# Kernel tuning notes

Hardware: AMD Instinct MI355X
Metric: run time of the kernel (lower is better)

The kernel has to match this reference:

```python
import jax, jax.numpy as jnp
import numpy as np

N_NODES = 100000
N_EDGES = 600000
NUM_GRAPHS = 512
IN_DIM = 128
HID = 64
HEADS = 2
NEG_SLOPE = 0.2


def gat_layer(h_in, src, dst, W, a_s, a_d, b, n_nodes):
    # W: [F_in, H*C], a_s/a_d: [H, C], b: [H*C]
    H, C = a_s.shape
    h = (h_in @ W).reshape(n_nodes, H, C)            # [N,H,C]
    alpha_src = jnp.einsum('nhc,hc->nh', h, a_s)      # [N,H]
    alpha_dst = jnp.einsum('nhc,hc->nh', h, a_d)      # [N,H]
    e = alpha_src[src] + alpha_dst[dst]               # [E,H]
    e = jnp.where(e >= 0, e, NEG_SLOPE * e)           # leaky_relu
    # segment softmax over destination node
    m = jax.ops.segment_max(e, dst, num_segments=n_nodes)
    m = jnp.where(jnp.isfinite(m), m, 0.0)
    ex = jnp.exp(e - m[dst])                          # [E,H]
    denom = jax.ops.segment_sum(ex, dst, num_segments=n_nodes)
    alpha = ex / jnp.maximum(denom[dst], 1e-16)       # [E,H]
    out = jax.ops.segment_sum(alpha[:, :, None] * h[src], dst, num_segments=n_nodes)
    return out.reshape(n_nodes, H * C) + b


def setup_inputs() -> dict:
    key = jax.random.key(0)
    ks = jax.random.split(key, 16)
    x = jax.random.normal(ks[0], (N_NODES, IN_DIM), dtype=jnp.float32)
    edge_index = jax.random.randint(ks[1], (2, N_EDGES), 0, N_NODES, dtype=jnp.int32)
    batch = jnp.sort(jax.random.randint(ks[2], (N_NODES,), 0, NUM_GRAPHS, dtype=jnp.int32))
    s = lambda *d: 1.0 / np.sqrt(d[0])
    W1 = jax.random.normal(ks[3], (IN_DIM, HEADS * HID), jnp.float32) * s(IN_DIM)
    a_src1 = jax.random.normal(ks[4], (HEADS, HID), jnp.float32) * s(HID)
    a_dst1 = jax.random.normal(ks[5], (HEADS, HID), jnp.float32) * s(HID)
    b1 = jnp.zeros((HEADS * HID,), jnp.float32)
    W2 = jax.random.normal(ks[6], (HEADS * HID, HID), jnp.float32) * s(HEADS * HID)
    a_src2 = jax.random.normal(ks[7], (1, HID), jnp.float32) * s(HID)
    a_dst2 = jax.random.normal(ks[8], (1, HID), jnp.float32) * s(HID)
    b2 = jnp.zeros((HID,), jnp.float32)
    Wf1 = jax.random.normal(ks[9], (2 * HID, HID), jnp.float32) * s(2 * HID)
    bf1 = jnp.zeros((HID,), jnp.float32)
    Wf2 = jax.random.normal(ks[10], (HID, 1), jnp.float32) * s(HID)
    bf2 = jnp.zeros((1,), jnp.float32)
    return dict(x=x, edge_index=edge_index, batch=batch, W1=W1, a_src1=a_src1,
                a_dst1=a_dst1, b1=b1, W2=W2, a_src2=a_src2, a_dst2=a_dst2, b2=b2,
                Wf1=Wf1, bf1=bf1, Wf2=Wf2, bf2=bf2)


def reference(x, edge_index, batch, W1, a_src1, a_dst1, b1, W2, a_src2, a_dst2, b2,
              Wf1, bf1, Wf2, bf2):
    n = x.shape[0]
    loops = jnp.arange(n, dtype=edge_index.dtype)
    src = jnp.concatenate([edge_index[0], loops])
    dst = jnp.concatenate([edge_index[1], loops])
    h = gat_layer(x, src, dst, W1, a_src1, a_dst1, b1, n)
    h = jax.nn.relu(h)
    h = gat_layer(h, src, dst, W2, a_src2, a_dst2, b2, n)  # [N, HID]
    # global mean + max pool per graph
    ones = jnp.ones((n,), h.dtype)
    counts = jax.ops.segment_sum(ones, batch, num_segments=NUM_GRAPHS)  # [G]
    mean = jax.ops.segment_sum(h, batch, num_segments=NUM_GRAPHS) / jnp.maximum(counts, 1.0)[:, None]
    mx = jax.ops.segment_max(h, batch, num_segments=NUM_GRAPHS)
    mx = jnp.where(counts[:, None] > 0, mx, 0.0)
    pooled = jnp.concatenate([mean, mx], axis=1)  # [G, 2*HID]
    out = jax.nn.relu(pooled @ Wf1 + bf1) @ Wf2 + bf2  # [G, 1]
    return out
```

## Files before the change

### kernel.cpp

```cpp
#include <hip/hip_runtime.h>

#define N_NODESC 100000
#define N_EDGESC 600000
#define E_TOTC   700000
#define NUM_GRAPHSC 512
#define NEG_SLOPE 0.2f
#define NEG_INF_ENC 0x007FFFFFu
#define SCAN_NB 128

typedef unsigned short ushort_t;
typedef __attribute__((ext_vector_type(8))) short bf16x8;
typedef __attribute__((ext_vector_type(4))) float f32x4;

__device__ __forceinline__ unsigned enc_f32(float f) {
    unsigned u = __float_as_uint(f);
    return (u & 0x80000000u) ? ~u : (u | 0x80000000u);
}
__device__ __forceinline__ float dec_f32(unsigned u) {
    u = (u & 0x80000000u) ? (u ^ 0x80000000u) : ~u;
    return __uint_as_float(u);
}
__device__ __forceinline__ ushort_t f32_to_bf16(float f) {
    unsigned u = __float_as_uint(f);
    return (ushort_t)((u + 0x7FFFu + ((u >> 16) & 1u)) >> 16);
}
__device__ __forceinline__ float bf16_to_f32(ushort_t h) {
    return __uint_as_float(((unsigned)h) << 16);
}
__device__ __forceinline__ unsigned pack_bf16x2(float a, float b) {
    return (unsigned)f32_to_bf16(a) | ((unsigned)f32_to_bf16(b) << 16);
}

__global__ __launch_bounds__(256) void init_all(float* __restrict__ msum,
                                                unsigned* __restrict__ mmax,
                                                float* __restrict__ cnt,
                                                int* __restrict__ deg,
                                                const float* __restrict__ W1,
                                                const float* __restrict__ W2,
                                                ushort_t* __restrict__ wPre1,
                                                ushort_t* __restrict__ wPre2) {
    int i = blockIdx.x * 256 + threadIdx.x;
    if (i < NUM_GRAPHSC * 64) { msum[i] = 0.f; mmax[i] = NEG_INF_ENC; }
    if (i < NUM_GRAPHSC) cnt[i] = 0.f;
    if (i < N_NODESC) deg[i] = 0;
    if (i < 128 * 128) {
        int n = i >> 7, k = i & 127;
        wPre1[n * 128 + k] = f32_to_bf16(W1[k * 128 + n]);
    } else if (i < 128 * 128 + 64 * 128) {
        int j = i - 128 * 128;
        int n = j >> 7, k = j & 127;
        wPre2[n * 128 + k] = f32_to_bf16(W2[k * 64 + n]);
    }
}

__global__ __launch_bounds__(256) void hist_dst(const int* __restrict__ ei,
                                                int* __restrict__ deg) {
    int e = blockIdx.x * blockDim.x + threadIdx.x;
    if (e >= E_TOTC) return;
    int d = (e < N_EDGESC) ? ei[N_EDGESC + e] : e - N_EDGESC;
    atomicAdd(&deg[d], 1);
}

__global__ __launch_bounds__(256) void scan_partial(const int* __restrict__ deg,
                                                    int* __restrict__ bsum, int n) {
    __shared__ int red[256];
    int chunk = (n + SCAN_NB - 1) / SCAN_NB;
    int lo = blockIdx.x * chunk, hi = min(lo + chunk, n);
    int s = 0;
    for (int i = lo + threadIdx.x; i < hi; i += 256) s += deg[i];
    red[threadIdx.x] = s;
    __syncthreads();
    for (int d = 128; d; d >>= 1) {
        if (threadIdx.x < d) red[threadIdx.x] += red[threadIdx.x + d];
        __syncthreads();
    }
    if (threadIdx.x == 0) bsum[blockIdx.x] = red[0];
}

__global__ __launch_bounds__(256) void scan_final(const int* __restrict__ deg,
                                                  const int* __restrict__ bsum,
                                                  int* __restrict__ off, int n) {
    __shared__ int bs[SCAN_NB];
    __shared__ int tile[256];
    __shared__ int carry;
    int t = threadIdx.x;
    if (t < SCAN_NB) bs[t] = bsum[t];
    __syncthreads();
    for (int d = 1; d < SCAN_NB; d <<= 1) {
        int v = (t >= d && t < SCAN_NB) ? bs[t - d] : 0;
        __syncthreads();
        if (t < SCAN_NB) bs[t] += v;
        __syncthreads();
    }
    if (t == 0) carry = blockIdx.x ? bs[blockIdx.x - 1] : 0;
    __syncthreads();
    int chunk = (n + SCAN_NB - 1) / SCAN_NB;
    int lo = blockIdx.x * chunk, hi = min(lo + chunk, n);
    for (int base = lo; base < hi; base += 256) {
        int i = base + t;
        int v = (i < hi) ? deg[i] : 0;
        tile[t] = v;
        __syncthreads();
        for (int d = 1; d < 256; d <<= 1) {
            int u = (t >= d) ? tile[t - d] : 0;
            __syncthreads();
            tile[t] += u;
            __syncthreads();
        }
        if (i < hi) off[i] = carry + tile[t] - v;
        __syncthreads();
        if (t == 0) carry += tile[255];
        __syncthreads();
    }
}

__global__ __launch_bounds__(256) void scatter_csr(const int* __restrict__ ei,
                                                   int* __restrict__ off,
                                                   int* __restrict__ csr) {
    int e = blockIdx.x * blockDim.x + threadIdx.x;
    if (e >= E_TOTC) return;
    int s, d;
    if (e < N_EDGESC) { s = ei[e]; d = ei[N_EDGESC + e]; } else { s = d = e - N_EDGESC; }
    int slot = atomicAdd(&off[d], 1);
    csr[slot] = s;
}

__global__ __launch_bounds__(256) void gemm1_mfma(const float* __restrict__ X,
                                                  const ushort_t* __restrict__ Wp,
                                                  ushort_t* __restrict__ Y16, int N) {
    int tid = threadIdx.x;
    int wave = tid >> 6, lane = tid & 63;
    int quad = lane >> 4, l16 = lane & 15;
    size_t node0 = (size_t)blockIdx.x * 64 + wave * 16;

    size_t arow = node0 + l16;
    if (arow >= (size_t)N) arow = N - 1;
    const float* xp = X + arow * 128;
    float4 xa[4], xb[4];
#pragma unroll
    for (int kc = 0; kc < 4; ++kc) {
        xa[kc] = *(const float4*)(xp + kc * 32 + quad * 8);
        xb[kc] = *(const float4*)(xp + kc * 32 + quad * 8 + 4);
    }

    f32x4 acc[8];
#pragma unroll
    for (int ct = 0; ct < 8; ++ct) acc[ct] = (f32x4){0.f, 0.f, 0.f, 0.f};

#pragma unroll
    for (int kc = 0; kc < 4; ++kc) {
        int kb = kc * 32 + quad * 8;
        union { bf16x8 v; unsigned u[4]; } af;
        af.u[0] = pack_bf16x2(xa[kc].x, xa[kc].y);
        af.u[1] = pack_bf16x2(xa[kc].z, xa[kc].w);
        af.u[2] = pack_bf16x2(xb[kc].x, xb[kc].y);
        af.u[3] = pack_bf16x2(xb[kc].z, xb[kc].w);
#pragma unroll
        for (int ct = 0; ct < 8; ++ct) {
            bf16x8 b = *(const bf16x8*)(Wp + (size_t)(ct * 16 + l16) * 128 + kb);
            acc[ct] = __builtin_amdgcn_mfma_f32_16x16x32_bf16(af.v, b, acc[ct], 0, 0, 0);
        }
    }
    unsigned* Yu = (unsigned*)Y16;
#pragma unroll
    for (int ct = 0; ct < 4; ++ct) {
        int c = ct * 16 + l16;
#pragma unroll
        for (int r = 0; r < 4; ++r) {
            size_t row = node0 + quad * 4 + r;
            if (row < (size_t)N)
                Yu[row * 64 + c] = pack_bf16x2(acc[ct][r], acc[ct + 4][r]);
        }
    }
}

__global__ __launch_bounds__(256) void gemm2_mfma(const ushort_t* __restrict__ Xb,
                                                  const ushort_t* __restrict__ Wp,
                                                  ushort_t* __restrict__ Y16, int N) {
    int tid = threadIdx.x;
    int wave = tid >> 6, lane = tid & 63;
    int quad = lane >> 4, l16 = lane & 15;
    int rbase = (wave >> 1) * 32, cbase = (wave & 1) * 32;
    size_t node0 = (size_t)blockIdx.x * 64;

    bf16x8 a[2][4];
#pragma unroll
    for (int rt = 0; rt < 2; ++rt) {
        size_t row = node0 + rbase + rt * 16 + l16;
        if (row >= (size_t)N) row = N - 1;
#pragma unroll
        for (int kc = 0; kc < 4; ++kc)
            a[rt][kc] = *(const bf16x8*)(Xb + row * 128 + kc * 32 + quad * 8);
    }

    const ushort_t* b0p = Wp + (size_t)(cbase + l16) * 128;
    const ushort_t* b1p = Wp + (size_t)(cbase + 16 + l16) * 128;

    f32x4 acc[2][2];
#pragma unroll
    for (int rt = 0; rt < 2; ++rt)
#pragma unroll
        for (int ct = 0; ct < 2; ++ct) acc[rt][ct] = (f32x4){0.f, 0.f, 0.f, 0.f};

#pragma unroll
    for (int kc = 0; kc < 4; ++kc) {
        int kb = kc * 32 + quad * 8;
        bf16x8 b0 = *(const bf16x8*)(b0p + kb);
        bf16x8 b1 = *(const bf16x8*)(b1p + kb);
#pragma unroll
        for (int rt = 0; rt < 2; ++rt) {
            acc[rt][0] = __builtin_amdgcn_mfma_f32_16x16x32_bf16(a[rt][kc], b0, acc[rt][0], 0, 0, 0);
            acc[rt][1] = __builtin_amdgcn_mfma_f32_16x16x32_bf16(a[rt][kc], b1, acc[rt][1], 0, 0, 0);
        }
    }
#pragma unroll
    for (int rt = 0; rt < 2; ++rt)
#pragma unroll
        for (int ct = 0; ct < 2; ++ct)
#pragma unroll
            for (int r = 0; r < 4; ++r) {
                size_t row = node0 + rbase + rt * 16 + quad * 4 + r;
                if (row < (size_t)N)
                    Y16[row * 64 + cbase + ct * 16 + l16] = f32_to_bf16(acc[rt][ct][r]);
            }
}

template <int H>
__global__ __launch_bounds__(256) void node_alpha(const ushort_t* __restrict__ H16,
                                                  const float* __restrict__ a_s,
                                                  const float* __restrict__ a_d,
                                                  float* __restrict__ as_out,
                                                  float* __restrict__ ad_out, int N) {
    int wid = threadIdx.x >> 6, lane = threadIdx.x & 63;
    int n = blockIdx.x * 4 + wid;
    if (n >= N) return;
    if (H == 2) {
        const unsigned* hrow = (const unsigned*)(H16 + (size_t)n * 128);
        unsigned u = hrow[lane];
        float h0 = __uint_as_float(u << 16);
        float h1 = __uint_as_float(u & 0xffff0000u);
        float ps0 = h0 * a_s[lane], pd0 = h0 * a_d[lane];
        float ps1 = h1 * a_s[64 + lane], pd1 = h1 * a_d[64 + lane];
#pragma unroll
        for (int off = 32; off; off >>= 1) {
            ps0 += __shfl_xor(ps0, off);
            pd0 += __shfl_xor(pd0, off);
            ps1 += __shfl_xor(ps1, off);
            pd1 += __shfl_xor(pd1, off);
        }
        if (lane == 0) {
            as_out[n * 2 + 0] = ps0; ad_out[n * 2 + 0] = pd0;
            as_out[n * 2 + 1] = ps1; ad_out[n * 2 + 1] = pd1;
        }
    } else {
        float hv = bf16_to_f32(H16[(size_t)n * 64 + lane]);
        float ps = hv * a_s[lane];
        float pd = hv * a_d[lane];
#pragma unroll
        for (int off = 32; off; off >>= 1) {
            ps += __shfl_xor(ps, off);
            pd += __shfl_xor(pd, off);
        }
        if (lane == 0) { as_out[n] = ps; ad_out[n] = pd; }
    }
}

template <int H, bool RELU, bool OB16>
__global__ __launch_bounds__(256) void gat_gather(const int* __restrict__ off_end,
                                                  const int* __restrict__ deg,
                                                  const int* __restrict__ csr,
                                                  const float* __restrict__ as,
                                                  const float* __restrict__ ad,
                                                  const ushort_t* __restrict__ H16,
                                                  const float* __restrict__ b,
                                                  void* __restrict__ outp, int N) {
    int lane = threadIdx.x & 63;
    int wave = threadIdx.x >> 6;
    int l = lane & 15;
    int gbase = lane & 48;
    int n = blockIdx.x * 16 + wave * 4 + (lane >> 4);
    if (n >= N) return;
    int dg = deg[n];
    int o = off_end[n] - dg;
    float adv[H];
#pragma unroll
    for (int h = 0; h < H; ++h) adv[h] = ad[n * H + h];

    float acc[H][4], den[H];
#pragma unroll
    for (int h = 0; h < H; ++h) {
        den[h] = 0.f;
#pragma unroll
        for (int q = 0; q < 4; ++q) acc[h][q] = 0.f;
    }

    const unsigned* Hu = (const unsigned*)H16;

    for (int base = 0; base < dg; base += 16) {
        int i = base + l;
        bool valid = i < dg;
        int s = valid ? csr[o + i] : 0;
        float v[H];
        if (H == 2) {
            float2 p = valid ? ((const float2*)as)[s] : make_float2(0.f, 0.f);
            v[0] = p.x + adv[0];
            v[H - 1] = p.y + adv[H - 1];
        } else {
            v[0] = valid ? as[s] + adv[0] : 0.f;
        }
#pragma unroll
        for (int h = 0; h < H; ++h) {
            float e = v[h] >= 0.f ? v[h] : NEG_SLOPE * v[h];
            v[h] = valid ? __expf(e) : 0.f;
            den[h] += v[h];
        }
        int wpk = (H == 2) ? (int)pack_bf16x2(v[0], v[H - 1])
                           : (int)__float_as_uint(v[0]);
        int cnt = min(dg - base, 16);
        int cnt4 = (cnt + 3) & ~3;
        for (int j = 0; j < cnt4; j += 4) {
#pragma unroll
            for (int u = 0; u < 4; ++u) {
                int src = gbase + j + u;
                int sj = __shfl(s, src);
                int wp = __shfl(wpk, src);
                if (H == 2) {
                    float w0 = __uint_as_float(((unsigned)wp) << 16);
                    float w1 = __uint_as_float(((unsigned)wp) & 0xffff0000u);
                    uint4 hu = *(const uint4*)(Hu + (size_t)sj * 64 + l * 4);
                    acc[0][0] += w0 * __uint_as_float(hu.x << 16);
                    acc[H - 1][0] += w1 * __uint_as_float(hu.x & 0xffff0000u);
                    acc[0][1] += w0 * __uint_as_float(hu.y << 16);
                    acc[H - 1][1] += w1 * __uint_as_float(hu.y & 0xffff0000u);
                    acc[0][2] += w0 * __uint_as_float(hu.z << 16);
                    acc[H - 1][2] += w1 * __uint_as_float(hu.z & 0xffff0000u);
                    acc[0][3] += w0 * __uint_as_float(hu.w << 16);
                    acc[H - 1][3] += w1 * __uint_as_float(hu.w & 0xffff0000u);
                } else {
                    float w0 = __uint_as_float((unsigned)wp);
                    uint2 hu = *(const uint2*)((const unsigned*)(H16 + (size_t)sj * 64) + l * 2);
                    acc[0][0] += w0 * __uint_as_float(hu.x << 16);
                    acc[0][1] += w0 * __uint_as_float(hu.x & 0xffff0000u);
                    acc[0][2] += w0 * __uint_as_float(hu.y << 16);
                    acc[0][3] += w0 * __uint_as_float(hu.y & 0xffff0000u);
                }
            }
        }
    }
#pragma unroll
    for (int h = 0; h < H; ++h) {
#pragma unroll
        for (int sh = 8; sh; sh >>= 1) den[h] += __shfl_xor(den[h], sh);
    }
    if (H == 2) {
        float4 b0 = *(const float4*)(b + l * 4);
        float4 b1 = *(const float4*)(b + 64 + l * 4);
        float r0[4], r1[4];
        float id0 = 1.f / fmaxf(den[0], 1e-16f);
        float id1 = 1.f / fmaxf(den[H - 1], 1e-16f);
        r0[0] = acc[0][0] * id0 + b0.x; r0[1] = acc[0][1] * id0 + b0.y;
        r0[2] = acc[0][2] * id0 + b0.z; r0[3] = acc[0][3] * id0 + b0.w;
        r1[0] = acc[H - 1][0] * id1 + b1.x; r1[1] = acc[H - 1][1] * id1 + b1.y;
        r1[2] = acc[H - 1][2] * id1 + b1.z; r1[3] = acc[H - 1][3] * id1 + b1.w;
        if (RELU) {
#pragma unroll
            for (int q = 0; q < 4; ++q) { r0[q] = fmaxf(r0[q], 0.f); r1[q] = fmaxf(r1[q], 0.f); }
        }
        ushort_t* outb = (ushort_t*)outp;
        uint2 p0 = make_uint2(pack_bf16x2(r0[0], r0[1]), pack_bf16x2(r0[2], r0[3]));
        uint2 p1 = make_uint2(pack_bf16x2(r1[0], r1[1]), pack_bf16x2(r1[2], r1[3]));
        *(uint2*)(outb + (size_t)n * 128 + l * 4) = p0;
        *(uint2*)(outb + (size_t)n * 128 + 64 + l * 4) = p1;
    } else {
        float4 bv = *(const float4*)(b + l * 4);
        float id0 = 1.f / fmaxf(den[0], 1e-16f);
        float4 r;
        r.x = acc[0][0] * id0 + bv.x; r.y = acc[0][1] * id0 + bv.y;
        r.z = acc[0][2] * id0 + bv.z; r.w = acc[0][3] * id0 + bv.w;
        if (RELU) { r.x = fmaxf(r.x, 0.f); r.y = fmaxf(r.y, 0.f);
                    r.z = fmaxf(r.z, 0.f); r.w = fmaxf(r.w, 0.f); }
        *(float4*)((float*)outp + (size_t)n * 64 + l * 4) = r;
    }
}

__global__ __launch_bounds__(256) void pool_nodes(const float* __restrict__ h2,
                                                  const int* __restrict__ batch,
                                                  float* __restrict__ msum,
                                                  unsigned* __restrict__ mmax,
                                                  float* __restrict__ cnt, int N) {
    int wid = threadIdx.x >> 6, lane = threadIdx.x & 63;
    int n0 = (blockIdx.x * 4 + wid) * 64;
    if (n0 >= N) return;
    int n1 = min(n0 + 64, N);
    int curg = batch[n0];
    float s = 0.f, m = -1e30f;
    int c = 0;
    for (int n = n0; n < n1; ++n) {
        int g = batch[n];
        float v = h2[(size_t)n * 64 + lane];
        if (g != curg) {
            atomicAdd(&msum[curg * 64 + lane], s);
            atomicMax(&mmax[curg * 64 + lane], enc_f32(m));
            if (lane == 0) atomicAdd(&cnt[curg], (float)c);
            s = 0.f; m = -1e30f; c = 0; curg = g;
        }
        s += v;
        m = fmaxf(m, v);
        ++c;
    }
    atomicAdd(&msum[curg * 64 + lane], s);
    atomicMax(&mmax[curg * 64 + lane], enc_f32(m));
    if (lane == 0) atomicAdd(&cnt[curg], (float)c);
}

__global__ __launch_bounds__(64) void mlp_head(const float* __restrict__ msum,
                                               const unsigned* __restrict__ mmax,
                                               const float* __restrict__ cnt,
                                               const float* __restrict__ Wf1,
                                               const float* __restrict__ bf1,
                                               const float* __restrict__ Wf2,
                                               const float* __restrict__ bf2,
                                               float* __restrict__ out) {
    __shared__ float pooled[128];
    int g = blockIdx.x, lane = threadIdx.x;
    float c = cnt[g];
    pooled[lane] = msum[g * 64 + lane] / fmaxf(c, 1.0f);
    pooled[64 + lane] = (c > 0.f) ? dec_f32(mmax[g * 64 + lane]) : 0.f;
    __syncthreads();
    float acc = bf1[lane];
#pragma unroll
    for (int k = 0; k < 128; ++k) acc += pooled[k] * Wf1[k * 64 + lane];
    acc = fmaxf(acc, 0.f);
    float r = acc * Wf2[lane];
#pragma unroll
    for (int off = 32; off; off >>= 1) r += __shfl_xor(r, off);
    if (lane == 0) out[g] = r + bf2[0];
}

extern "C" void kernel_launch(void* const* d_in, const int* in_sizes, int n_in,
                              void* d_out, int out_size, void* d_ws, size_t ws_size,
                              hipStream_t stream) {
    const float* x    = (const float*)d_in[0];
    const int*   ei   = (const int*)d_in[1];
    const int*   batch= (const int*)d_in[2];
    const float* W1   = (const float*)d_in[3];
    const float* as1  = (const float*)d_in[4];
    const float* ad1  = (const float*)d_in[5];
    const float* b1   = (const float*)d_in[6];
    const float* W2   = (const float*)d_in[7];
    const float* as2  = (const float*)d_in[8];
    const float* ad2  = (const float*)d_in[9];
    const float* b2   = (const float*)d_in[10];
    const float* Wf1  = (const float*)d_in[11];
    const float* bf1  = (const float*)d_in[12];
    const float* Wf2  = (const float*)d_in[13];
    const float* bf2  = (const float*)d_in[14];
    float* out = (float*)d_out;

    const size_t N = N_NODESC;
    float* ws = (float*)d_ws;
    ushort_t* h16_1 = (ushort_t*)ws;
    ushort_t* out1b = (ushort_t*)(ws + N * 64);
    ushort_t* h16_2 = (ushort_t*)(ws + N * 128);
    float*    out2  = ws + N * 160;
    float*    small = ws + N * 224;
    float*    as1b = small;
    float*    ad1b = small + 2 * N;
    float*    as2b = small + 4 * N;
    float*    ad2b = small + 5 * N;
    float*    msum = small + 6 * N;
    unsigned* mmax = (unsigned*)(small + 6 * N + 512 * 64);
    float*    cntb = small + 6 * N + 2 * 512 * 64;
    int* ip  = (int*)(small + 6 * N + 2 * 512 * 64 + 512);
    int* deg  = ip;
    int* off  = ip + N;
    int* csr  = ip + 2 * N;
    int* bsum = ip + 2 * N + E_TOTC;
    ushort_t* wPre1 = (ushort_t*)(bsum + SCAN_NB);
    ushort_t* wPre2 = wPre1 + 128 * 128;

    init_all<<<(N_NODESC + 255) / 256, 256, 0, stream>>>(msum, mmax, cntb, deg,
                                                         W1, W2, wPre1, wPre2);

    hist_dst<<<(E_TOTC + 255) / 256, 256, 0, stream>>>(ei, deg);
    scan_partial<<<SCAN_NB, 256, 0, stream>>>(deg, bsum, N);
    scan_final<<<SCAN_NB, 256, 0, stream>>>(deg, bsum, off, N);
    scatter_csr<<<(E_TOTC + 255) / 256, 256, 0, stream>>>(ei, off, csr);

    const int NBLK64 = (N_NODESC + 63) / 64;
    const int NBLK16 = (N_NODESC + 15) / 16;

    gemm1_mfma<<<NBLK64, 256, 0, stream>>>(x, wPre1, h16_1, N);
    node_alpha<2><<<(N + 3) / 4, 256, 0, stream>>>(h16_1, as1, ad1, as1b, ad1b, N);
    gat_gather<2, true, true><<<NBLK16, 256, 0, stream>>>(off, deg, csr, as1b,
                                                          ad1b, h16_1, b1, out1b, N);

    gemm2_mfma<<<NBLK64, 256, 0, stream>>>(out1b, wPre2, h16_2, N);
    node_alpha<1><<<(N + 3) / 4, 256, 0, stream>>>(h16_2, as2, ad2, as2b, ad2b, N);
    gat_gather<1, false, false><<<NBLK16, 256, 0, stream>>>(off, deg, csr, as2b,
                                                            ad2b, h16_2, b2, out2, N);

    pool_nodes<<<(N + 255) / 256, 256, 0, stream>>>(out2, batch, msum, mmax, cntb, N);
    mlp_head<<<NUM_GRAPHSC, 64, 0, stream>>>(msum, mmax, cntb, Wf1, bf1, Wf2, bf2, out);
}
```

Baseline: 345.0 us.

## Fuse attention-score dot products into MFMA GEMM epilogues via atomics

Removes the separate node_alpha kernels and computes per-node source/destination attention scores inside the GEMM epilogues. Each wave reduces a 16-column slice with shuffles and adds it into zero-initialised alpha buffers with float atomics. To make this work the GEMMs are re-tiled to 16 nodes per block, with each wave owning a column slice. The fusion saves two launches and a re-read of the bf16 features, at the cost of atomics, extra zeroing work in init, and four times as many GEMM blocks that each reload the A rows.

```diff
diff --git a/kernel.cpp b/kernel.cpp
--- a/kernel.cpp
+++ b/kernel.cpp
@@ -38,11 +38,13 @@
                                                 const float* __restrict__ W1,
                                                 const float* __restrict__ W2,
                                                 ushort_t* __restrict__ wPre1,
-                                                ushort_t* __restrict__ wPre2) {
+                                                ushort_t* __restrict__ wPre2,
+                                                float* __restrict__ alphas) {
     int i = blockIdx.x * 256 + threadIdx.x;
     if (i < NUM_GRAPHSC * 64) { msum[i] = 0.f; mmax[i] = NEG_INF_ENC; }
     if (i < NUM_GRAPHSC) cnt[i] = 0.f;
     if (i < N_NODESC) deg[i] = 0;
+    if (i < 6 * N_NODESC) alphas[i] = 0.f;
     if (i < 128 * 128) {
         int n = i >> 7, k = i & 127;
         wPre1[n * 128 + k] = f32_to_bf16(W1[k * 128 + n]);
@@ -127,11 +129,15 @@
 
 __global__ __launch_bounds__(256) void gemm1_mfma(const float* __restrict__ X,
                                                   const ushort_t* __restrict__ Wp,
+                                                  const float* __restrict__ a_s,
+                                                  const float* __restrict__ a_d,
+                                                  float* __restrict__ as_out,
+                                                  float* __restrict__ ad_out,
                                                   ushort_t* __restrict__ Y16, int N) {
     int tid = threadIdx.x;
     int wave = tid >> 6, lane = tid & 63;
     int quad = lane >> 4, l16 = lane & 15;
-    size_t node0 = (size_t)blockIdx.x * 64 + wave * 16;
+    size_t node0 = (size_t)blockIdx.x * 16;
 
     size_t arow = node0 + l16;
     if (arow >= (size_t)N) arow = N - 1;
@@ -143,9 +149,11 @@
         xb[kc] = *(const float4*)(xp + kc * 32 + quad * 8 + 4);
     }
 
-    f32x4 acc[8];
-#pragma unroll
-    for (int ct = 0; ct < 8; ++ct) acc[ct] = (f32x4){0.f, 0.f, 0.f, 0.f};
+    const ushort_t* bp0 = Wp + (size_t)(wave * 16 + l16) * 128;
+    const ushort_t* bp1 = Wp + (size_t)((wave + 4) * 16 + l16) * 128;
+
+    f32x4 acc0 = (f32x4){0.f, 0.f, 0.f, 0.f};
+    f32x4 acc1 = (f32x4){0.f, 0.f, 0.f, 0.f};
 
 #pragma unroll
     for (int kc = 0; kc < 4; ++kc) {
@@ -155,113 +163,85 @@
         af.u[1] = pack_bf16x2(xa[kc].z, xa[kc].w);
         af.u[2] = pack_bf16x2(xb[kc].x, xb[kc].y);
         af.u[3] = pack_bf16x2(xb[kc].z, xb[kc].w);
-#pragma unroll
-        for (int ct = 0; ct < 8; ++ct) {
-            bf16x8 b = *(const bf16x8*)(Wp + (size_t)(ct * 16 + l16) * 128 + kb);
-            acc[ct] = __builtin_amdgcn_mfma_f32_16x16x32_bf16(af.v, b, acc[ct], 0, 0, 0);
-        }
-    }
+        bf16x8 b0 = *(const bf16x8*)(bp0 + kb);
+        bf16x8 b1 = *(const bf16x8*)(bp1 + kb);
+        acc0 = __builtin_amdgcn_mfma_f32_16x16x32_bf16(af.v, b0, acc0, 0, 0, 0);
+        acc1 = __builtin_amdgcn_mfma_f32_16x16x32_bf16(af.v, b1, acc1, 0, 0, 0);
+    }
+
     unsigned* Yu = (unsigned*)Y16;
-#pragma unroll
-    for (int ct = 0; ct < 4; ++ct) {
-        int c = ct * 16 + l16;
-#pragma unroll
-        for (int r = 0; r < 4; ++r) {
-            size_t row = node0 + quad * 4 + r;
-            if (row < (size_t)N)
-                Yu[row * 64 + c] = pack_bf16x2(acc[ct][r], acc[ct + 4][r]);
+    int c = wave * 16 + l16;
+    float as0v = a_s[c], as1v = a_s[64 + c];
+    float ad0v = a_d[c], ad1v = a_d[64 + c];
+#pragma unroll
+    for (int r = 0; r < 4; ++r) {
+        size_t row = node0 + quad * 4 + r;
+        bool ok = row < (size_t)N;
+        if (ok) Yu[row * 64 + c] = pack_bf16x2(acc0[r], acc1[r]);
+        float ps = acc0[r] * as0v, pd = acc0[r] * ad0v;
+        float qs = acc1[r] * as1v, qd = acc1[r] * ad1v;
+#pragma unroll
+        for (int sh = 1; sh < 16; sh <<= 1) {
+            ps += __shfl_xor(ps, sh);
+            pd += __shfl_xor(pd, sh);
+            qs += __shfl_xor(qs, sh);
+            qd += __shfl_xor(qd, sh);
+        }
+        if (l16 == 0 && ok) {
+            atomicAdd(&as_out[row * 2 + 0], ps);
+            atomicAdd(&ad_out[row * 2 + 0], pd);
+            atomicAdd(&as_out[row * 2 + 1], qs);
+            atomicAdd(&ad_out[row * 2 + 1], qd);
         }
     }
 }
 
 __global__ __launch_bounds__(256) void gemm2_mfma(const ushort_t* __restrict__ Xb,
                                                   const ushort_t* __restrict__ Wp,
+                                                  const float* __restrict__ a_s,
+                                                  const float* __restrict__ a_d,
+                                                  float* __restrict__ as_out,
+                                                  float* __restrict__ ad_out,
                                                   ushort_t* __restrict__ Y16, int N) {
     int tid = threadIdx.x;
     int wave = tid >> 6, lane = tid & 63;
     int quad = lane >> 4, l16 = lane & 15;
-    int rbase = (wave >> 1) * 32, cbase = (wave & 1) * 32;
-    size_t node0 = (size_t)blockIdx.x * 64;
-
-    bf16x8 a[2][4];
-#pragma unroll
-    for (int rt = 0; rt < 2; ++rt) {
-        size_t row = node0 + rbase + rt * 16 + l16;
-        if (row >= (size_t)N) row = N - 1;
-#pragma unroll
-        for (int kc = 0; kc < 4; ++kc)
-            a[rt][kc] = *(const bf16x8*)(Xb + row * 128 + kc * 32 + quad * 8);
-    }
-
-    const ushort_t* b0p = Wp + (size_t)(cbase + l16) * 128;
-    const ushort_t* b1p = Wp + (size_t)(cbase + 16 + l16) * 128;
-
-    f32x4 acc[2][2];
-#pragma unroll
-    for (int rt = 0; rt < 2; ++rt)
-#pragma unroll
-        for (int ct = 0; ct < 2; ++ct) acc[rt][ct] = (f32x4){0.f, 0.f, 0.f, 0.f};
-
+    size_t node0 = (size_t)blockIdx.x * 16;
+
+    size_t arow = node0 + l16;
+    if (arow >= (size_t)N) arow = N - 1;
+    const ushort_t* xp = Xb + arow * 128;
+    bf16x8 a[4];
+#pragma unroll
+    for (int kc = 0; kc < 4; ++kc)
+        a[kc] = *(const bf16x8*)(xp + kc * 32 + quad * 8);
+
+    const ushort_t* bp = Wp + (size_t)(wave * 16 + l16) * 128;
+    f32x4 acc = (f32x4){0.f, 0.f, 0.f, 0.f};
 #pragma unroll
     for (int kc = 0; kc < 4; ++kc) {
         int kb = kc * 32 + quad * 8;
-        bf16x8 b0 = *(const bf16x8*)(b0p + kb);
-        bf16x8 b1 = *(const bf16x8*)(b1p + kb);
-#pragma unroll
-        for (int rt = 0; rt < 2; ++rt) {
-            acc[rt][0] = __builtin_amdgcn_mfma_f32_16x16x32_bf16(a[rt][kc], b0, acc[rt][0], 0, 0, 0);
-            acc[rt][1] = __builtin_amdgcn_mfma_f32_16x16x32_bf16(a[rt][kc], b1, acc[rt][1], 0, 0, 0);
-        }
-    }
-#pragma unroll
-    for (int rt = 0; rt < 2; ++rt)
-#pragma unroll
-        for (int ct = 0; ct < 2; ++ct)
-#pragma unroll
-            for (int r = 0; r < 4; ++r) {
-                size_t row = node0 + rbase + rt * 16 + quad * 4 + r;
-                if (row < (size_t)N)
-                    Y16[row * 64 + cbase + ct * 16 + l16] = f32_to_bf16(acc[rt][ct][r]);
-            }
-}
-
-template <int H>
-__global__ __launch_bounds__(256) void node_alpha(const ushort_t* __restrict__ H16,
-                                                  const float* __restrict__ a_s,
-                                                  const float* __restrict__ a_d,
-                                                  float* __restrict__ as_out,
-                                                  float* __restrict__ ad_out, int N) {
-    int wid = threadIdx.x >> 6, lane = threadIdx.x & 63;
-    int n = blockIdx.x * 4 + wid;
-    if (n >= N) return;
-    if (H == 2) {
-        const unsigned* hrow = (const unsigned*)(H16 + (size_t)n * 128);
-        unsigned u = hrow[lane];
-        float h0 = __uint_as_float(u << 16);
-        float h1 = __uint_as_float(u & 0xffff0000u);
-        float ps0 = h0 * a_s[lane], pd0 = h0 * a_d[lane];
-        float ps1 = h1 * a_s[64 + lane], pd1 = h1 * a_d[64 + lane];
-#pragma unroll
-        for (int off = 32; off; off >>= 1) {
-            ps0 += __shfl_xor(ps0, off);
-            pd0 += __shfl_xor(pd0, off);
-            ps1 += __shfl_xor(ps1, off);
-            pd1 += __shfl_xor(pd1, off);
-        }
-        if (lane == 0) {
-            as_out[n * 2 + 0] = ps0; ad_out[n * 2 + 0] = pd0;
-            as_out[n * 2 + 1] = ps1; ad_out[n * 2 + 1] = pd1;
-        }
-    } else {
-        float hv = bf16_to_f32(H16[(size_t)n * 64 + lane]);
-        float ps = hv * a_s[lane];
-        float pd = hv * a_d[lane];
-#pragma unroll
-        for (int off = 32; off; off >>= 1) {
-            ps += __shfl_xor(ps, off);
-            pd += __shfl_xor(pd, off);
-        }
-        if (lane == 0) { as_out[n] = ps; ad_out[n] = pd; }
+        bf16x8 b = *(const bf16x8*)(bp + kb);
+        acc = __builtin_amdgcn_mfma_f32_16x16x32_bf16(a[kc], b, acc, 0, 0, 0);
+    }
+
+    int c = wave * 16 + l16;
+    float asv = a_s[c], adv = a_d[c];
+#pragma unroll
+    for (int r = 0; r < 4; ++r) {
+        size_t row = node0 + quad * 4 + r;
+        bool ok = row < (size_t)N;
+        if (ok) Y16[row * 64 + c] = f32_to_bf16(acc[r]);
+        float ps = acc[r] * asv, pd = acc[r] * adv;
+#pragma unroll
+        for (int sh = 1; sh < 16; sh <<= 1) {
+            ps += __shfl_xor(ps, sh);
+            pd += __shfl_xor(pd, sh);
+        }
+        if (l16 == 0 && ok) {
+            atomicAdd(&as_out[row], ps);
+            atomicAdd(&ad_out[row], pd);
+        }
     }
 }
 
@@ -479,26 +459,24 @@
     ushort_t* wPre1 = (ushort_t*)(bsum + SCAN_NB);
     ushort_t* wPre2 = wPre1 + 128 * 128;
 
-    init_all<<<(N_NODESC + 255) / 256, 256, 0, stream>>>(msum, mmax, cntb, deg,
-                                                         W1, W2, wPre1, wPre2);
+    init_all<<<(6 * N_NODESC + 255) / 256, 256, 0, stream>>>(msum, mmax, cntb, deg,
+                                                             W1, W2, wPre1, wPre2,
+                                                             small);
 
     hist_dst<<<(E_TOTC + 255) / 256, 256, 0, stream>>>(ei, deg);
     scan_partial<<<SCAN_NB, 256, 0, stream>>>(deg, bsum, N);
     scan_final<<<SCAN_NB, 256, 0, stream>>>(deg, bsum, off, N);
     scatter_csr<<<(E_TOTC + 255) / 256, 256, 0, stream>>>(ei, off, csr);
 
-    const int NBLK64 = (N_NODESC + 63) / 64;
-    const int NBLK16 = (N_NODESC + 15) / 16;
-
-    gemm1_mfma<<<NBLK64, 256, 0, stream>>>(x, wPre1, h16_1, N);
-    node_alpha<2><<<(N + 3) / 4, 256, 0, stream>>>(h16_1, as1, ad1, as1b, ad1b, N);
-    gat_gather<2, true, true><<<NBLK16, 256, 0, stream>>>(off, deg, csr, as1b,
-                                                          ad1b, h16_1, b1, out1b, N);
-
-    gemm2_mfma<<<NBLK64, 256, 0, stream>>>(out1b, wPre2, h16_2, N);
-    node_alpha<1><<<(N + 3) / 4, 256, 0, stream>>>(h16_2, as2, ad2, as2b, ad2b, N);
-    gat_gather<1, false, false><<<NBLK16, 256, 0, stream>>>(off, deg, csr, as2b,
-                                                            ad2b, h16_2, b2, out2, N);
+    const int NBLK16G = (N_NODESC + 15) / 16;
+
+    gemm1_mfma<<<NBLK16G, 256, 0, stream>>>(x, wPre1, as1, ad1, as1b, ad1b, h16_1, N);
+    gat_gather<2, true, true><<<NBLK16G, 256, 0, stream>>>(off, deg, csr, as1b,
+                                                           ad1b, h16_1, b1, out1b, N);
+
+    gemm2_mfma<<<NBLK16G, 256, 0, stream>>>(out1b, wPre2, as2, ad2, as2b, ad2b, h16_2, N);
+    gat_gather<1, false, false><<<NBLK16G, 256, 0, stream>>>(off, deg, csr, as2b,
+                                                             ad2b, h16_2, b2, out2, N);
 
     pool_nodes<<<(N + 255) / 256, 256, 0, stream>>>(out2, batch, msum, mmax, cntb, N);
     mlp_head<<<NUM_GRAPHSC, 64, 0, stream>>>(msum, mmax, cntb, Wf1, bf1, Wf2, bf2, out);
```

After: 332.1 us. 3.7% less time.

## Fuse attention logits into GEMM epilogues and stage inputs via LDS

Applied to the files above, without the earlier changes.

The per-node attention dot products (alpha_src/alpha_dst) are now computed in the MFMA GEMM epilogues from fp32 accumulators. This removes the two node_alpha launches and their re-read of the bf16 feature rows. Both GEMMs now stage their input rows into swizzled LDS with global_load_lds, and gemm2 is restructured so each wave owns 16 rows across all 64 columns. The cost is a larger LDS footprint (32KB in gemm1), which may lower occupancy. Logits also now come from unrounded fp32 values instead of bf16, a small numerical difference.

```diff
diff --git a/kernel.cpp b/kernel.cpp
--- a/kernel.cpp
+++ b/kernel.cpp
@@ -29,6 +29,12 @@
 }
 __device__ __forceinline__ unsigned pack_bf16x2(float a, float b) {
     return (unsigned)f32_to_bf16(a) | ((unsigned)f32_to_bf16(b) << 16);
+}
+
+__device__ __forceinline__ void glds16(const void* g, void* l) {
+    __builtin_amdgcn_global_load_lds(
+        (const __attribute__((address_space(1))) void*)g,
+        (__attribute__((address_space(3))) void*)l, 16, 0, 0);
 }
 
 __global__ __launch_bounds__(256) void init_all(float* __restrict__ msum,
@@ -127,141 +133,161 @@
 
 __global__ __launch_bounds__(256) void gemm1_mfma(const float* __restrict__ X,
                                                   const ushort_t* __restrict__ Wp,
+                                                  const float* __restrict__ a_s,
+                                                  const float* __restrict__ a_d,
+                                                  float* __restrict__ as_out,
+                                                  float* __restrict__ ad_out,
                                                   ushort_t* __restrict__ Y16, int N) {
+    __shared__ float sx[64 * 128];
     int tid = threadIdx.x;
     int wave = tid >> 6, lane = tid & 63;
     int quad = lane >> 4, l16 = lane & 15;
-    size_t node0 = (size_t)blockIdx.x * 64 + wave * 16;
-
-    size_t arow = node0 + l16;
-    if (arow >= (size_t)N) arow = N - 1;
-    const float* xp = X + arow * 128;
-    float4 xa[4], xb[4];
+    size_t node0 = (size_t)blockIdx.x * 64 + (size_t)wave * 16;
+
+    {
+        int rhalf = lane >> 5;
+        int cb = (lane & 31) * 16;
+#pragma unroll
+        for (int c = 0; c < 8; ++c) {
+            int rl = 2 * c + rhalf;
+            size_t grow = node0 + rl;
+            if (grow >= (size_t)N) grow = N - 1;
+            int goff = cb ^ ((rl & 15) << 4);
+            glds16((const char*)(X + grow * 128) + goff,
+                   (char*)sx + wave * 8192 + c * 1024);
+        }
+    }
+    asm volatile("s_waitcnt vmcnt(0)" ::: "memory");
+    __builtin_amdgcn_sched_barrier(0);
+
+    const char* swx = (const char*)sx + wave * 8192 + l16 * 512;
+    int skey = (l16 & 15) << 4;
+
+    f32x4 acc[8];
+#pragma unroll
+    for (int ct = 0; ct < 8; ++ct) acc[ct] = (f32x4){0.f, 0.f, 0.f, 0.f};
+
 #pragma unroll
     for (int kc = 0; kc < 4; ++kc) {
-        xa[kc] = *(const float4*)(xp + kc * 32 + quad * 8);
-        xb[kc] = *(const float4*)(xp + kc * 32 + quad * 8 + 4);
-    }
-
-    f32x4 acc[8];
-#pragma unroll
-    for (int ct = 0; ct < 8; ++ct) acc[ct] = (f32x4){0.f, 0.f, 0.f, 0.f};
-
-#pragma unroll
-    for (int kc = 0; kc < 4; ++kc) {
-        int kb = kc * 32 + quad * 8;
+        int b = kc * 128 + quad * 32;
+        float4 xa = *(const float4*)(swx + (b ^ skey));
+        float4 xb = *(const float4*)(swx + ((b + 16) ^ skey));
         union { bf16x8 v; unsigned u[4]; } af;
-        af.u[0] = pack_bf16x2(xa[kc].x, xa[kc].y);
-        af.u[1] = pack_bf16x2(xa[kc].z, xa[kc].w);
-        af.u[2] = pack_bf16x2(xb[kc].x, xb[kc].y);
-        af.u[3] = pack_bf16x2(xb[kc].z, xb[kc].w);
+        af.u[0] = pack_bf16x2(xa.x, xa.y);
+        af.u[1] = pack_bf16x2(xa.z, xa.w);
+        af.u[2] = pack_bf16x2(xb.x, xb.y);
+        af.u[3] = pack_bf16x2(xb.z, xb.w);
 #pragma unroll
         for (int ct = 0; ct < 8; ++ct) {
-            bf16x8 b = *(const bf16x8*)(Wp + (size_t)(ct * 16 + l16) * 128 + kb);
-            acc[ct] = __builtin_amdgcn_mfma_f32_16x16x32_bf16(af.v, b, acc[ct], 0, 0, 0);
-        }
-    }
+            bf16x8 bb = *(const bf16x8*)(Wp + (size_t)(ct * 16 + l16) * 128 + kc * 32 + quad * 8);
+            acc[ct] = __builtin_amdgcn_mfma_f32_16x16x32_bf16(af.v, bb, acc[ct], 0, 0, 0);
+        }
+    }
+
     unsigned* Yu = (unsigned*)Y16;
+    float asv0[4], asv1[4], adv0[4], adv1[4];
 #pragma unroll
     for (int ct = 0; ct < 4; ++ct) {
         int c = ct * 16 + l16;
-#pragma unroll
-        for (int r = 0; r < 4; ++r) {
-            size_t row = node0 + quad * 4 + r;
-            if (row < (size_t)N)
-                Yu[row * 64 + c] = pack_bf16x2(acc[ct][r], acc[ct + 4][r]);
+        asv0[ct] = a_s[c]; asv1[ct] = a_s[64 + c];
+        adv0[ct] = a_d[c]; adv1[ct] = a_d[64 + c];
+    }
+#pragma unroll
+    for (int r = 0; r < 4; ++r) {
+        size_t row = node0 + quad * 4 + r;
+        bool ok = row < (size_t)N;
+        if (ok) {
+#pragma unroll
+            for (int ct = 0; ct < 4; ++ct)
+                Yu[row * 64 + ct * 16 + l16] = pack_bf16x2(acc[ct][r], acc[ct + 4][r]);
+        }
+        float ps0 = 0.f, pd0 = 0.f, ps1 = 0.f, pd1 = 0.f;
+#pragma unroll
+        for (int ct = 0; ct < 4; ++ct) {
+            ps0 += acc[ct][r] * asv0[ct];     pd0 += acc[ct][r] * adv0[ct];
+            ps1 += acc[ct + 4][r] * asv1[ct]; pd1 += acc[ct + 4][r] * adv1[ct];
+        }
+#pragma unroll
+        for (int sh = 1; sh < 16; sh <<= 1) {
+            ps0 += __shfl_xor(ps0, sh); pd0 += __shfl_xor(pd0, sh);
+            ps1 += __shfl_xor(ps1, sh); pd1 += __shfl_xor(pd1, sh);
+        }
+        if (l16 == 0 && ok) {
+            *(float2*)(as_out + row * 2) = make_float2(ps0, ps1);
+            *(float2*)(ad_out + row * 2) = make_float2(pd0, pd1);
         }
     }
 }
 
 __global__ __launch_bounds__(256) void gemm2_mfma(const ushort_t* __restrict__ Xb,
                                                   const ushort_t* __restrict__ Wp,
+                                                  const float* __restrict__ a_s,
+                                                  const float* __restrict__ a_d,
+                                                  float* __restrict__ as_out,
+                                                  float* __restrict__ ad_out,
                                                   ushort_t* __restrict__ Y16, int N) {
+    __shared__ ushort_t sx[64 * 128];
     int tid = threadIdx.x;
     int wave = tid >> 6, lane = tid & 63;
     int quad = lane >> 4, l16 = lane & 15;
-    int rbase = (wave >> 1) * 32, cbase = (wave & 1) * 32;
-    size_t node0 = (size_t)blockIdx.x * 64;
-
-    bf16x8 a[2][4];
-#pragma unroll
-    for (int rt = 0; rt < 2; ++rt) {
-        size_t row = node0 + rbase + rt * 16 + l16;
-        if (row >= (size_t)N) row = N - 1;
-#pragma unroll
-        for (int kc = 0; kc < 4; ++kc)
-            a[rt][kc] = *(const bf16x8*)(Xb + row * 128 + kc * 32 + quad * 8);
-    }
-
-    const ushort_t* b0p = Wp + (size_t)(cbase + l16) * 128;
-    const ushort_t* b1p = Wp + (size_t)(cbase + 16 + l16) * 128;
-
-    f32x4 acc[2][2];
-#pragma unroll
-    for (int rt = 0; rt < 2; ++rt)
-#pragma unroll
-        for (int ct = 0; ct < 2; ++ct) acc[rt][ct] = (f32x4){0.f, 0.f, 0.f, 0.f};
+    size_t node0 = (size_t)blockIdx.x * 64 + (size_t)wave * 16;
+
+    {
+        int rq = lane >> 4;
+        int cb = (lane & 15) * 16;
+#pragma unroll
+        for (int c = 0; c < 4; ++c) {
+            int rl = 4 * c + rq;
+            size_t grow = node0 + rl;
+            if (grow >= (size_t)N) grow = N - 1;
+            int goff = cb ^ ((rl & 15) << 4);
+            glds16((const char*)(Xb + grow * 128) + goff,
+                   (char*)sx + wave * 4096 + c * 1024);
+        }
+    }
+    asm volatile("s_waitcnt vmcnt(0)" ::: "memory");
+    __builtin_amdgcn_sched_barrier(0);
+
+    const char* swx = (const char*)sx + wave * 4096 + l16 * 256;
+    int skey = (l16 & 15) << 4;
+
+    f32x4 acc[4];
+#pragma unroll
+    for (int ct = 0; ct < 4; ++ct) acc[ct] = (f32x4){0.f, 0.f, 0.f, 0.f};
 
 #pragma unroll
     for (int kc = 0; kc < 4; ++kc) {
-        int kb = kc * 32 + quad * 8;
-        bf16x8 b0 = *(const bf16x8*)(b0p + kb);
-        bf16x8 b1 = *(const bf16x8*)(b1p + kb);
-#pragma unroll
-        for (int rt = 0; rt < 2; ++rt) {
-            acc[rt][0] = __builtin_amdgcn_mfma_f32_16x16x32_bf16(a[rt][kc], b0, acc[rt][0], 0, 0, 0);
-            acc[rt][1] = __builtin_amdgcn_mfma_f32_16x16x32_bf16(a[rt][kc], b1, acc[rt][1], 0, 0, 0);
-        }
-    }
-#pragma unroll
-    for (int rt = 0; rt < 2; ++rt)
-#pragma unroll
-        for (int ct = 0; ct < 2; ++ct)
-#pragma unroll
-            for (int r = 0; r < 4; ++r) {
-                size_t row = node0 + rbase + rt * 16 + quad * 4 + r;
-                if (row < (size_t)N)
-                    Y16[row * 64 + cbase + ct * 16 + l16] = f32_to_bf16(acc[rt][ct][r]);
-            }
-}
-
-template <int H>
-__global__ __launch_bounds__(256) void node_alpha(const ushort_t* __restrict__ H16,
-                                                  const float* __restrict__ a_s,
-                                                  const float* __restrict__ a_d,
-                                                  float* __restrict__ as_out,
-                                                  float* __restrict__ ad_out, int N) {
-    int wid = threadIdx.x >> 6, lane = threadIdx.x & 63;
-    int n = blockIdx.x * 4 + wid;
-    if (n >= N) return;
-    if (H == 2) {
-        const unsigned* hrow = (const unsigned*)(H16 + (size_t)n * 128);
-        unsigned u = hrow[lane];
-        float h0 = __uint_as_float(u << 16);
-        float h1 = __uint_as_float(u & 0xffff0000u);
-        float ps0 = h0 * a_s[lane], pd0 = h0 * a_d[lane];
-        float ps1 = h1 * a_s[64 + lane], pd1 = h1 * a_d[64 + lane];
-#pragma unroll
-        for (int off = 32; off; off >>= 1) {
-            ps0 += __shfl_xor(ps0, off);
-            pd0 += __shfl_xor(pd0, off);
-            ps1 += __shfl_xor(ps1, off);
-            pd1 += __shfl_xor(pd1, off);
-        }
-        if (lane == 0) {
-            as_out[n * 2 + 0] = ps0; ad_out[n * 2 + 0] = pd0;
-            as_out[n * 2 + 1] = ps1; ad_out[n * 2 + 1] = pd1;
-        }
-    } else {
-        float hv = bf16_to_f32(H16[(size_t)n * 64 + lane]);
-        float ps = hv * a_s[lane];
-        float pd = hv * a_d[lane];
-#pragma unroll
-        for (int off = 32; off; off >>= 1) {
-            ps += __shfl_xor(ps, off);
-            pd += __shfl_xor(pd, off);
-        }
-        if (lane == 0) { as_out[n] = ps; ad_out[n] = pd; }
+        int b = kc * 64 + quad * 16;
+        bf16x8 a = *(const bf16x8*)(swx + (b ^ skey));
+#pragma unroll
+        for (int ct = 0; ct < 4; ++ct) {
+            bf16x8 bb = *(const bf16x8*)(Wp + (size_t)(ct * 16 + l16) * 128 + kc * 32 + quad * 8);
+            acc[ct] = __builtin_amdgcn_mfma_f32_16x16x32_bf16(a, bb, acc[ct], 0, 0, 0);
+        }
+    }
+
+    float asv[4], adv[4];
+#pragma unroll
+    for (int ct = 0; ct < 4; ++ct) { asv[ct] = a_s[ct * 16 + l16]; adv[ct] = a_d[ct * 16 + l16]; }
+#pragma unroll
+    for (int r = 0; r < 4; ++r) {
+        size_t row = node0 + quad * 4 + r;
+        bool ok = row < (size_t)N;
+        if (ok) {
+#pragma unroll
+            for (int ct = 0; ct < 4; ++ct)
+                Y16[row * 64 + ct * 16 + l16] = f32_to_bf16(acc[ct][r]);
+        }
+        float ps = acc[0][r] * asv[0] + acc[1][r] * asv[1] +
+                   acc[2][r] * asv[2] + acc[3][r] * asv[3];
+        float pd = acc[0][r] * adv[0] + acc[1][r] * adv[1] +
+                   acc[2][r] * adv[2] + acc[3][r] * adv[3];
+#pragma unroll
+        for (int sh = 1; sh < 16; sh <<= 1) {
+            ps += __shfl_xor(ps, sh);
+            pd += __shfl_xor(pd, sh);
+        }
+        if (l16 == 0 && ok) { as_out[row] = ps; ad_out[row] = pd; }
     }
 }
 
@@ -490,13 +516,11 @@
     const int NBLK64 = (N_NODESC + 63) / 64;
     const int NBLK16 = (N_NODESC + 15) / 16;
 
-    gemm1_mfma<<<NBLK64, 256, 0, stream>>>(x, wPre1, h16_1, N);
-    node_alpha<2><<<(N + 3) / 4, 256, 0, stream>>>(h16_1, as1, ad1, as1b, ad1b, N);
+    gemm1_mfma<<<NBLK64, 256, 0, stream>>>(x, wPre1, as1, ad1, as1b, ad1b, h16_1, N);
     gat_gather<2, true, true><<<NBLK16, 256, 0, stream>>>(off, deg, csr, as1b,
                                                           ad1b, h16_1, b1, out1b, N);
 
-    gemm2_mfma<<<NBLK64, 256, 0, stream>>>(out1b, wPre2, h16_2, N);
-    node_alpha<1><<<(N + 3) / 4, 256, 0, stream>>>(h16_2, as2, ad2, as2b, ad2b, N);
+    gemm2_mfma<<<NBLK64, 256, 0, stream>>>(out1b, wPre2, as2, ad2, as2b, ad2b, h16_2, N);
     gat_gather<1, false, false><<<NBLK16, 256, 0, stream>>>(off, deg, csr, as2b,
                                                             ad2b, h16_2, b2, out2, N);
 
```

New measurement: 305.1 us. 11.5% less time.
